# Kernel tuning notes

Measured on AMD Instinct MI355X. Metric: run time of the kernel, lower is better.

## Reference

```python
import jax, jax.numpy as jnp
import numpy as np

B, N_E, E_DIM = 131072, 1024, 64
BETA = 0.25


def setup_inputs() -> dict:
    key = jax.random.key(0)
    kz, kw = jax.random.split(key)
    z = jax.random.normal(kz, (B, E_DIM), dtype=jnp.float32)
    # nn.Embedding init: uniform(-1/n_e, 1/n_e)
    emb_w = jax.random.uniform(kw, (N_E, E_DIM), dtype=jnp.float32,
                               minval=-1.0 / N_E, maxval=1.0 / N_E)
    return {"z": z, "emb_w": emb_w}


def reference(z, emb_w):
    beta = jnp.float32(BETA)
    # pairwise squared distances: [B, n_e]
    d = (jnp.sum(z * z, axis=1, keepdims=True)
         + jnp.sum(emb_w * emb_w, axis=1)
         - 2.0 * jnp.einsum('bd,nd->bn', z, emb_w))
    idx = jnp.argmin(d, axis=1)                      # [B]
    z_q = jnp.take(emb_w, idx, axis=0)               # [B, e_dim]
    # legacy=False branch
    loss = (beta * jnp.mean((jax.lax.stop_gradient(z_q) - z) ** 2)
            + jnp.mean((z_q - jax.lax.stop_gradient(z)) ** 2))
    # straight-through estimator
    z_q_st = z + jax.lax.stop_gradient(z_q - z)
    # torch.var is unbiased (ddof=1)
    v = jnp.var(idx.astype(jnp.float32), ddof=1)
    return (z_q_st, loss, idx, v)
```

## Files before the change

### kernel.cpp

```cpp
#include <hip/hip_runtime.h>
#include <stdint.h>


typedef __attribute__((ext_vector_type(8))) __bf16 bf16x8;
typedef __attribute__((ext_vector_type(4))) float f32x4;

#define OUT_LOSS 8388608
#define OUT_IDX  8388609
#define OUT_VAR  8519681

#define WS_LOSS  0
#define WS_S1    8192
#define WS_S2    16384
#define WS_EFRAG 24576
#define WS_EE    155648

__device__ __forceinline__ void gld_lds16(const void* g, void* l) {
  __builtin_amdgcn_global_load_lds(
      (const __attribute__((address_space(1))) unsigned*)g,
      (__attribute__((address_space(3))) unsigned*)l, 16, 0, 0);
}

__global__ void vq_prep(const float* __restrict__ emb, char* __restrict__ ws) {
  bf16x8* efrag = (bf16x8*)(ws + WS_EFRAG);
  float* eeoff = (float*)(ws + WS_EE);
  const int t = blockIdx.x;
  const int l = threadIdx.x;
  const int n = t * 16 + (l & 15);
  const int kb0 = (l >> 4) * 8;
  const float* er = emb + n * 64;
  for (int j = 0; j < 2; ++j) {
    const int kb = j * 32 + kb0;
    bf16x8 h;
#pragma unroll
    for (int i = 0; i < 8; ++i) h[i] = (__bf16)(-2.0f * er[kb + i]);
    efrag[(t * 2 + j) * 64 + l] = h;
  }
  if (l < 16) {
    const float* e2 = emb + (t * 16 + l) * 64;
    float s = 0.f;
#pragma unroll
    for (int d = 0; d < 64; ++d) s += e2[d] * e2[d];
    eeoff[t * 16 + l] = s + 0.5f;
  }
}

__global__ void __launch_bounds__(256) vq_main(
    const float* __restrict__ z, const float* __restrict__ emb,
    float* __restrict__ out, char* __restrict__ ws) {
  __shared__ char smfrag[2][4][4096];
  __shared__ float see[1024];
  __shared__ unsigned skey[4][64];
  __shared__ float szz[64];
  __shared__ float sL[4];
  __shared__ int sA[4], sB[4];

  const int tid = threadIdx.x;
  const int wave = tid >> 6, lane = tid & 63;
  const int lr = lane & 15, ksl = lane >> 4;
  const int k0 = ksl * 8;
  const int row_base = blockIdx.x * 64;

#define STAGE(p, b)                                                            \
  {                                                                            \
    _Pragma("unroll")                                                          \
    for (int i_ = 0; i_ < 4; ++i_)                                             \
      gld_lds16(ws + WS_EFRAG + (size_t)(wave * 16 + (p) * 2) * 2048           \
                    + i_ * 1024 + lane * 16,                                   \
                smfrag[b][wave] + i_ * 1024);                                  \
  }

  f32x4 zr[16];
#pragma unroll
  for (int r = 0; r < 4; ++r) {
    const float* zp = z + (size_t)(row_base + r * 16 + lr) * 64;
    zr[r * 4 + 0] = *(const f32x4*)(zp + k0);
    zr[r * 4 + 1] = *(const f32x4*)(zp + k0 + 4);
    zr[r * 4 + 2] = *(const f32x4*)(zp + 32 + k0);
    zr[r * 4 + 3] = *(const f32x4*)(zp + 32 + k0 + 4);
  }

  gld_lds16(ws + WS_EE + wave * 1024 + lane * 16, (char*)see + wave * 1024);
  STAGE(0, 0);
  STAGE(1, 1);

  bf16x8 zf[4][2];
#pragma unroll
  for (int r = 0; r < 4; ++r) {
#pragma unroll
    for (int i = 0; i < 4; ++i) {
      zf[r][0][i] = (__bf16)zr[r * 4 + 0][i]; zf[r][0][4 + i] = (__bf16)zr[r * 4 + 1][i];
      zf[r][1][i] = (__bf16)zr[r * 4 + 2][i]; zf[r][1][4 + i] = (__bf16)zr[r * 4 + 3][i];
    }
  }
  if (wave == 0) {
#pragma unroll
    for (int r = 0; r < 4; ++r) {
      float s = 0.f;
#pragma unroll
      for (int i = 0; i < 4; ++i)
        s += zr[r * 4 + 0][i] * zr[r * 4 + 0][i] + zr[r * 4 + 1][i] * zr[r * 4 + 1][i]
           + zr[r * 4 + 2][i] * zr[r * 4 + 2][i] + zr[r * 4 + 3][i] * zr[r * 4 + 3][i];
      s += __shfl_xor(s, 16, 64);
      s += __shfl_xor(s, 32, 64);
      if (ksl == 0) szz[r * 16 + lr] = s;
    }
  }

  unsigned rk[4];
#pragma unroll
  for (int r = 0; r < 4; ++r) rk[r] = 0xFFFFFFFFu;
  const unsigned kj0 = (unsigned)(ksl * 4), kj1 = kj0 + 1, kj2 = kj0 + 2, kj3 = kj0 + 3;

  for (int ph = 0; ph < 8; ++ph) {
    if (ph < 7) { asm volatile("s_waitcnt vmcnt(4)" ::: "memory"); }
    else        { asm volatile("s_waitcnt vmcnt(0)" ::: "memory"); }
    __builtin_amdgcn_sched_barrier(0);
    const bf16x8* sf = (const bf16x8*)(smfrag[ph & 1][wave]);
    __builtin_amdgcn_s_setprio(1);
#pragma unroll
    for (int t2 = 0; t2 < 2; ++t2) {
      const int g = wave * 16 + ph * 2 + t2;
      bf16x8 e0 = sf[(t2 * 2 + 0) * 64 + lane];
      bf16x8 e1 = sf[(t2 * 2 + 1) * 64 + lane];
      const f32x4 ee = *(const f32x4*)(see + g * 16 + ksl * 4);
      const unsigned g16 = (unsigned)(g * 16);
#pragma unroll
      for (int r = 0; r < 4; ++r) {
        f32x4 a = __builtin_amdgcn_mfma_f32_16x16x32_bf16(e0, zf[r][0], ee, 0, 0, 0);
        a = __builtin_amdgcn_mfma_f32_16x16x32_bf16(e1, zf[r][1], a, 0, 0, 0);
        const unsigned t0 = (__float_as_uint(a[0]) & 0xFFFFFC00u) | kj0;
        const unsigned t1 = (__float_as_uint(a[1]) & 0xFFFFFC00u) | kj1;
        const unsigned t2k = (__float_as_uint(a[2]) & 0xFFFFFC00u) | kj2;
        const unsigned t3 = (__float_as_uint(a[3]) & 0xFFFFFC00u) | kj3;
        rk[r] = min(rk[r], min(min(min(t0, t1), t2k), t3) + g16);
      }
    }
    __builtin_amdgcn_s_setprio(0);
    if (ph < 6) STAGE(ph + 2, ph & 1);
  }
#undef STAGE

#pragma unroll
  for (int r = 0; r < 4; ++r) {
    rk[r] = min(rk[r], (unsigned)__shfl_xor((int)rk[r], 16, 64));
    rk[r] = min(rk[r], (unsigned)__shfl_xor((int)rk[r], 32, 64));
  }
  if (ksl == 0) {
#pragma unroll
    for (int r = 0; r < 4; ++r) skey[wave][r * 16 + lr] = rk[r];
  }
  __syncthreads();

  const int row = tid >> 2, seg = tid & 3;
  const unsigned k = min(min(skey[0][row], skey[1][row]),
                         min(skey[2][row], skey[3][row]));
  const unsigned idx = k & 1023u;
  const size_t rowg = (size_t)row_base + row;
  const f32x4* ep = (const f32x4*)(emb + (size_t)idx * 64 + seg * 16);
  f32x4* op = (f32x4*)(out + rowg * 64 + seg * 16);
#pragma unroll
  for (int c = 0; c < 4; ++c) op[c] = ep[c];

  float ls = 0.f; int s1 = 0, s2 = 0;
  if (seg == 0) {
    ls = szz[row] + __uint_as_float(k & 0xFFFFFC00u) - 0.5f;
    s1 = (int)idx;
    s2 = (int)(idx * idx);
    out[OUT_IDX + rowg] = (float)idx;
  }
#pragma unroll
  for (int off = 1; off < 64; off <<= 1) {
    ls += __shfl_xor(ls, off, 64);
    s1 += __shfl_xor(s1, off, 64);
    s2 += __shfl_xor(s2, off, 64);
  }
  if (lane == 0) { sL[wave] = ls; sA[wave] = s1; sB[wave] = s2; }
  __syncthreads();
  if (tid == 0) {
    float L = 0; int a = 0, b = 0;
#pragma unroll
    for (int w = 0; w < 4; ++w) { L += sL[w]; a += sA[w]; b += sB[w]; }
    ((float*)(ws + WS_LOSS))[blockIdx.x] = L;
    ((int*)(ws + WS_S1))[blockIdx.x] = a;
    ((int*)(ws + WS_S2))[blockIdx.x] = b;
  }
}

__global__ void vq_final(float* __restrict__ out, const char* __restrict__ ws) {
  const int t = threadIdx.x;
  const float* lp = (const float*)(ws + WS_LOSS);
  const int* p1 = (const int*)(ws + WS_S1);
  const int* p2 = (const int*)(ws + WS_S2);
  double L = 0; long long a = 0, b = 0;
#pragma unroll
  for (int kk = 0; kk < 8; ++kk) {
    const int i = t + 256 * kk;
    L += (double)lp[i];
    a += (long long)p1[i];
    b += (long long)p2[i];
  }
#pragma unroll
  for (int off = 1; off < 64; off <<= 1) {
    L += __shfl_xor(L, off, 64);
    a += __shfl_xor(a, off, 64);
    b += __shfl_xor(b, off, 64);
  }
  __shared__ double sLf[4];
  __shared__ long long sAf[4], sBf[4];
  const int wave = t >> 6, lane = t & 63;
  if (lane == 0) { sLf[wave] = L; sAf[wave] = a; sBf[wave] = b; }
  __syncthreads();
  if (t == 0) {
    double Lt = 0; long long at = 0, bt = 0;
#pragma unroll
    for (int w = 0; w < 4; ++w) { Lt += sLf[w]; at += sAf[w]; bt += sBf[w]; }
    out[OUT_LOSS] = (float)(1.25 * Lt / 8388608.0);
    long long num = bt * 131072LL - at * at;
    out[OUT_VAR] = (float)((double)num / (131072.0 * 131071.0));
  }
}

extern "C" void kernel_launch(void* const* d_in, const int* in_sizes, int n_in,
                              void* d_out, int out_size, void* d_ws, size_t ws_size,
                              hipStream_t stream) {
  (void)in_sizes; (void)n_in; (void)out_size; (void)ws_size;
  const float* z = (const float*)d_in[0];
  const float* emb = (const float*)d_in[1];
  float* out = (float*)d_out;
  char* ws = (char*)d_ws;
  vq_prep<<<64, 64, 0, stream>>>(emb, ws);
  vq_main<<<2048, 256, 0, stream>>>(z, emb, out, ws);
  vq_final<<<1, 256, 0, stream>>>(out, ws);
}
```

Baseline: 49.04 us.

## Split VQ into codebook-half distance kernel and separate gather/output kernel

Replaces the fused main kernel with two kernels. The first has each block keep half of the codebook fragments (64KB) resident in LDS, and each wave processes 128 rows against that half. It writes per-row partial argmin keys and squared norms to the workspace. A second kernel merges the two half keys per row, gathers the codeword, writes the outputs and does the per-block reductions. This removes the repeated per-block streaming of the full codebook through double-buffered LDS, at the cost of an extra launch, a global round trip for the keys, and lower occupancy from the large LDS allocation.

```diff
diff --git a/kernel.cpp b/kernel.cpp
--- a/kernel.cpp
+++ b/kernel.cpp
@@ -14,6 +14,8 @@
 #define WS_S2    16384
 #define WS_EFRAG 24576
 #define WS_EE    155648
+#define WS_KEY   159744
+#define WS_ZZ    1208320
 
 __device__ __forceinline__ void gld_lds16(const void* g, void* l) {
   __builtin_amdgcn_global_load_lds(
@@ -45,118 +47,127 @@
   }
 }
 
-__global__ void __launch_bounds__(256) vq_main(
-    const float* __restrict__ z, const float* __restrict__ emb,
-    float* __restrict__ out, char* __restrict__ ws) {
-  __shared__ char smfrag[2][4][4096];
-  __shared__ float see[1024];
-  __shared__ unsigned skey[4][64];
-  __shared__ float szz[64];
-  __shared__ float sL[4];
-  __shared__ int sA[4], sB[4];
+__global__ void __launch_bounds__(256) vq_dist(
+    const float* __restrict__ z, char* __restrict__ ws) {
+  __shared__ char sfrag[65536];
+  __shared__ float see[512];
 
   const int tid = threadIdx.x;
   const int wave = tid >> 6, lane = tid & 63;
   const int lr = lane & 15, ksl = lane >> 4;
   const int k0 = ksl * 8;
-  const int row_base = blockIdx.x * 64;
-
-#define STAGE(p, b)                                                            \
-  {                                                                            \
-    _Pragma("unroll")                                                          \
-    for (int i_ = 0; i_ < 4; ++i_)                                             \
-      gld_lds16(ws + WS_EFRAG + (size_t)(wave * 16 + (p) * 2) * 2048           \
-                    + i_ * 1024 + lane * 16,                                   \
-                smfrag[b][wave] + i_ * 1024);                                  \
-  }
+  const int half = blockIdx.x & 1;
+  const int rb0 = (blockIdx.x >> 1) * 512 + wave * 64;
+
+  unsigned* wkey = (unsigned*)(ws + WS_KEY);
+  float* wzz = (float*)(ws + WS_ZZ);
 
   f32x4 zr[16];
 #pragma unroll
   for (int r = 0; r < 4; ++r) {
-    const float* zp = z + (size_t)(row_base + r * 16 + lr) * 64;
+    const float* zp = z + (size_t)(rb0 + r * 16 + lr) * 64;
     zr[r * 4 + 0] = *(const f32x4*)(zp + k0);
     zr[r * 4 + 1] = *(const f32x4*)(zp + k0 + 4);
     zr[r * 4 + 2] = *(const f32x4*)(zp + 32 + k0);
     zr[r * 4 + 3] = *(const f32x4*)(zp + 32 + k0 + 4);
   }
 
-  gld_lds16(ws + WS_EE + wave * 1024 + lane * 16, (char*)see + wave * 1024);
-  STAGE(0, 0);
-  STAGE(1, 1);
-
-  bf16x8 zf[4][2];
-#pragma unroll
-  for (int r = 0; r < 4; ++r) {
-#pragma unroll
-    for (int i = 0; i < 4; ++i) {
-      zf[r][0][i] = (__bf16)zr[r * 4 + 0][i]; zf[r][0][4 + i] = (__bf16)zr[r * 4 + 1][i];
-      zf[r][1][i] = (__bf16)zr[r * 4 + 2][i]; zf[r][1][4 + i] = (__bf16)zr[r * 4 + 3][i];
-    }
-  }
-  if (wave == 0) {
+#pragma unroll
+  for (int i = 0; i < 16; ++i)
+    gld_lds16(ws + WS_EFRAG + half * 65536 + i * 4096 + wave * 1024 + lane * 16,
+              sfrag + i * 4096 + wave * 1024);
+  if (wave < 2)
+    gld_lds16(ws + WS_EE + half * 2048 + wave * 1024 + lane * 16,
+              (char*)see + wave * 1024);
+  asm volatile("s_waitcnt vmcnt(0)" ::: "memory");
+  __syncthreads();
+
+  const bf16x8* sf = (const bf16x8*)sfrag;
+  const unsigned kj0 = (unsigned)(ksl * 4), kj1 = kj0 + 1, kj2 = kj0 + 2, kj3 = kj0 + 3;
+
+#pragma unroll
+  for (int it = 0; it < 2; ++it) {
+    const int rbase = rb0 + it * 256;
+    bf16x8 zf[4][2];
+    float zz[4];
 #pragma unroll
     for (int r = 0; r < 4; ++r) {
       float s = 0.f;
 #pragma unroll
-      for (int i = 0; i < 4; ++i)
+      for (int i = 0; i < 4; ++i) {
+        zf[r][0][i] = (__bf16)zr[r * 4 + 0][i]; zf[r][0][4 + i] = (__bf16)zr[r * 4 + 1][i];
+        zf[r][1][i] = (__bf16)zr[r * 4 + 2][i]; zf[r][1][4 + i] = (__bf16)zr[r * 4 + 3][i];
         s += zr[r * 4 + 0][i] * zr[r * 4 + 0][i] + zr[r * 4 + 1][i] * zr[r * 4 + 1][i]
            + zr[r * 4 + 2][i] * zr[r * 4 + 2][i] + zr[r * 4 + 3][i] * zr[r * 4 + 3][i];
+      }
       s += __shfl_xor(s, 16, 64);
       s += __shfl_xor(s, 32, 64);
-      if (ksl == 0) szz[r * 16 + lr] = s;
-    }
-  }
-
-  unsigned rk[4];
-#pragma unroll
-  for (int r = 0; r < 4; ++r) rk[r] = 0xFFFFFFFFu;
-  const unsigned kj0 = (unsigned)(ksl * 4), kj1 = kj0 + 1, kj2 = kj0 + 2, kj3 = kj0 + 3;
-
-  for (int ph = 0; ph < 8; ++ph) {
-    if (ph < 7) { asm volatile("s_waitcnt vmcnt(4)" ::: "memory"); }
-    else        { asm volatile("s_waitcnt vmcnt(0)" ::: "memory"); }
-    __builtin_amdgcn_sched_barrier(0);
-    const bf16x8* sf = (const bf16x8*)(smfrag[ph & 1][wave]);
-    __builtin_amdgcn_s_setprio(1);
-#pragma unroll
-    for (int t2 = 0; t2 < 2; ++t2) {
-      const int g = wave * 16 + ph * 2 + t2;
-      bf16x8 e0 = sf[(t2 * 2 + 0) * 64 + lane];
-      bf16x8 e1 = sf[(t2 * 2 + 1) * 64 + lane];
-      const f32x4 ee = *(const f32x4*)(see + g * 16 + ksl * 4);
-      const unsigned g16 = (unsigned)(g * 16);
+      zz[r] = s;
+    }
+    if (it == 0) {
+#pragma unroll
+      for (int r = 0; r < 4; ++r) {
+        const float* zp = z + (size_t)(rb0 + 256 + r * 16 + lr) * 64;
+        zr[r * 4 + 0] = *(const f32x4*)(zp + k0);
+        zr[r * 4 + 1] = *(const f32x4*)(zp + k0 + 4);
+        zr[r * 4 + 2] = *(const f32x4*)(zp + 32 + k0);
+        zr[r * 4 + 3] = *(const f32x4*)(zp + 32 + k0 + 4);
+      }
+    }
+
+    unsigned rk[4];
+#pragma unroll
+    for (int r = 0; r < 4; ++r) rk[r] = 0xFFFFFFFFu;
+
+#pragma unroll 4
+    for (int tt = 0; tt < 32; ++tt) {
+      bf16x8 e0 = sf[(tt * 2 + 0) * 64 + lane];
+      bf16x8 e1 = sf[(tt * 2 + 1) * 64 + lane];
+      const f32x4 ee = *(const f32x4*)(see + tt * 16 + ksl * 4);
+      const unsigned g16 = (unsigned)((half * 32 + tt) * 16);
 #pragma unroll
       for (int r = 0; r < 4; ++r) {
         f32x4 a = __builtin_amdgcn_mfma_f32_16x16x32_bf16(e0, zf[r][0], ee, 0, 0, 0);
         a = __builtin_amdgcn_mfma_f32_16x16x32_bf16(e1, zf[r][1], a, 0, 0, 0);
         const unsigned t0 = (__float_as_uint(a[0]) & 0xFFFFFC00u) | kj0;
         const unsigned t1 = (__float_as_uint(a[1]) & 0xFFFFFC00u) | kj1;
-        const unsigned t2k = (__float_as_uint(a[2]) & 0xFFFFFC00u) | kj2;
+        const unsigned t2 = (__float_as_uint(a[2]) & 0xFFFFFC00u) | kj2;
         const unsigned t3 = (__float_as_uint(a[3]) & 0xFFFFFC00u) | kj3;
-        rk[r] = min(rk[r], min(min(min(t0, t1), t2k), t3) + g16);
-      }
-    }
-    __builtin_amdgcn_s_setprio(0);
-    if (ph < 6) STAGE(ph + 2, ph & 1);
-  }
-#undef STAGE
-
-#pragma unroll
-  for (int r = 0; r < 4; ++r) {
-    rk[r] = min(rk[r], (unsigned)__shfl_xor((int)rk[r], 16, 64));
-    rk[r] = min(rk[r], (unsigned)__shfl_xor((int)rk[r], 32, 64));
-  }
-  if (ksl == 0) {
-#pragma unroll
-    for (int r = 0; r < 4; ++r) skey[wave][r * 16 + lr] = rk[r];
-  }
-  __syncthreads();
-
+        rk[r] = min(rk[r], min(min(t0, t1), min(t2, t3)) + g16);
+      }
+    }
+
+#pragma unroll
+    for (int r = 0; r < 4; ++r) {
+      rk[r] = min(rk[r], (unsigned)__shfl_xor((int)rk[r], 16, 64));
+      rk[r] = min(rk[r], (unsigned)__shfl_xor((int)rk[r], 32, 64));
+    }
+    if (ksl == 0) {
+#pragma unroll
+      for (int r = 0; r < 4; ++r) {
+        const int rowg = rbase + r * 16 + lr;
+        wkey[(size_t)rowg * 2 + half] = rk[r];
+        if (half == 0) wzz[rowg] = zz[r];
+      }
+    }
+  }
+}
+
+__global__ void __launch_bounds__(256) vq_out(
+    const float* __restrict__ emb, float* __restrict__ out,
+    char* __restrict__ ws) {
+  const int tid = threadIdx.x;
+  const int wave = tid >> 6, lane = tid & 63;
   const int row = tid >> 2, seg = tid & 3;
-  const unsigned k = min(min(skey[0][row], skey[1][row]),
-                         min(skey[2][row], skey[3][row]));
+  const size_t rowg = (size_t)blockIdx.x * 64 + row;
+
+  const unsigned* wkey = (const unsigned*)(ws + WS_KEY);
+  const float* wzz = (const float*)(ws + WS_ZZ);
+
+  const uint2 kk = ((const uint2*)wkey)[rowg];
+  const unsigned k = min(kk.x, kk.y);
   const unsigned idx = k & 1023u;
-  const size_t rowg = (size_t)row_base + row;
+
   const f32x4* ep = (const f32x4*)(emb + (size_t)idx * 64 + seg * 16);
   f32x4* op = (f32x4*)(out + rowg * 64 + seg * 16);
 #pragma unroll
@@ -164,7 +175,7 @@
 
   float ls = 0.f; int s1 = 0, s2 = 0;
   if (seg == 0) {
-    ls = szz[row] + __uint_as_float(k & 0xFFFFFC00u) - 0.5f;
+    ls = wzz[rowg] + __uint_as_float(k & 0xFFFFFC00u) - 0.5f;
     s1 = (int)idx;
     s2 = (int)(idx * idx);
     out[OUT_IDX + rowg] = (float)idx;
@@ -175,6 +186,8 @@
     s1 += __shfl_xor(s1, off, 64);
     s2 += __shfl_xor(s2, off, 64);
   }
+  __shared__ float sL[4];
+  __shared__ int sA[4], sB[4];
   if (lane == 0) { sL[wave] = ls; sA[wave] = s1; sB[wave] = s2; }
   __syncthreads();
   if (tid == 0) {
@@ -230,6 +243,7 @@
   float* out = (float*)d_out;
   char* ws = (char*)d_ws;
   vq_prep<<<64, 64, 0, stream>>>(emb, ws);
-  vq_main<<<2048, 256, 0, stream>>>(z, emb, out, ws);
+  vq_dist<<<512, 256, 0, stream>>>(z, ws);
+  vq_out<<<2048, 256, 0, stream>>>(emb, out, ws);
   vq_final<<<1, 256, 0, stream>>>(out, ws);
 }
```

Result: slower. 54.31 us (+10.8%).
